# Kernel optimization log

Measured on AMD Instinct MI355X. Metric: run time of the kernel, lower is better.

## Reference

```python
import jax, jax.numpy as jnp
import numpy as np

N_NODES = 8   # chain DAG 0->1->...->7
B = 2048      # n_samples
T_STEPS = 8   # end_wind
Z_DIM = 32    # latent_dim // 2
EMB = 8       # emb_dim
GRU_H = 24
HID = 64


def setup_inputs() -> dict:
    key = jax.random.key(0)
    ks = jax.random.split(key, 20)
    def rn(k, shape, scale=0.1):
        return jax.random.normal(k, shape, jnp.float32) * scale
    return {
        "z": jax.random.normal(ks[0], (N_NODES, B, T_STEPS, Z_DIM), jnp.float32),
        "cond_w1": rn(ks[1], (N_NODES, 32, 1)),
        "cond_b1": rn(ks[2], (N_NODES, 32)),
        "cond_w2": rn(ks[3], (N_NODES, EMB, 32)),
        "cond_b2": rn(ks[4], (N_NODES, EMB)),
        "proj_w": rn(ks[5], (N_NODES, GRU_H, Z_DIM + 2 * EMB)),  # node 0 uses first 40 cols
        "proj_b": rn(ks[6], (N_NODES, GRU_H)),
        "gru_proj_w": rn(ks[7], (GRU_H, GRU_H)),
        "gru_proj_b": rn(ks[8], (GRU_H,)),
        "gru_wih": rn(ks[9], (N_NODES, 2, 3 * GRU_H, GRU_H)),
        "gru_whh": rn(ks[10], (N_NODES, 2, 3 * GRU_H, GRU_H)),
        "gru_bih": rn(ks[11], (N_NODES, 2, 3 * GRU_H)),
        "gru_bhh": rn(ks[12], (N_NODES, 2, 3 * GRU_H)),
        "cm_w1": rn(ks[13], (N_NODES, HID, GRU_H)),
        "cm_b1": rn(ks[14], (N_NODES, HID)),
        "cm_w2": rn(ks[15], (N_NODES, HID, HID)),
        "cm_b2": rn(ks[16], (N_NODES, HID)),
        "cm_w3": rn(ks[17], (N_NODES, 1, HID)),
        "cm_b3": rn(ks[18], (N_NODES, 1)),
        "end_wind": T_STEPS,
    }


def _leaky(x):
    return jnp.where(x >= 0, x, 0.01 * x)  # nn.LeakyReLU default slope


def _gru_layer(x, wih, whh, bih, bhh):
    """torch nn.GRU single layer, batch_first. x: [B, L, H] -> [B, L, H]."""
    h0 = jnp.zeros((x.shape[0], GRU_H), x.dtype)
    def step(h, xt):
        gi = xt @ wih.T + bih            # [B, 3H], gate order r, z, n
        gh = h @ whh.T + bhh
        i_r, i_z, i_n = jnp.split(gi, 3, axis=-1)
        h_r, h_z, h_n = jnp.split(gh, 3, axis=-1)
        r = jax.nn.sigmoid(i_r + h_r)
        zg = jax.nn.sigmoid(i_z + h_z)
        n = jnp.tanh(i_n + r * h_n)
        hn = (1.0 - zg) * n + zg * h
        return hn, hn
    _, ys = jax.lax.scan(step, h0, jnp.swapaxes(x, 0, 1))
    return jnp.swapaxes(ys, 0, 1)


def _forward(z, cond_w1, cond_b1, cond_w2, cond_b2, proj_w, proj_b,
             gru_proj_w, gru_proj_b, gru_wih, gru_whh, gru_bih, gru_bhh,
             cm_w1, cm_b1, cm_w2, cm_b2, cm_w3, cm_b3, end_wind):
    n_nodes, bsz = z.shape[0], z.shape[1]
    dt = z.dtype

    def cond_net(n, x):  # x: [B, L, 1] -> [B, L, EMB]
        h = jax.nn.relu(x @ cond_w1[n].T + cond_b1[n])
        return h @ cond_w2[n].T + cond_b2[n]

    def pipeline(n, z_mod):  # decode_pipeline: proj -> leaky -> gru_proj -> 2-layer GRU -> CausalMap
        w = proj_w[n][:, : z_mod.shape[-1]]
        h = _leaky(z_mod @ w.T + proj_b[n])
        g = h @ gru_proj_w.T + gru_proj_b
        y = _gru_layer(g, gru_wih[n, 0], gru_whh[n, 0], gru_bih[n, 0], gru_bhh[n, 0])
        y = _gru_layer(y, gru_wih[n, 1], gru_whh[n, 1], gru_bih[n, 1], gru_bhh[n, 1])
        d = jax.nn.relu(y @ cm_w1[n].T + cm_b1[n])
        d = jax.nn.relu(d @ cm_w2[n].T + cm_b2[n])
        return d @ cm_w3[n].T + cm_b3[n]  # [B, L, 1]

    decoded = [None] * n_nodes
    reals = [[] for _ in range(n_nodes)]
    for idx in range(end_wind):
        # chain DAG: in-degree grouping (deg 0 = node 0, deg 1 = nodes 1..7 in order)
        # coincides with node order 0..N-1.
        for node in range(n_nodes):
            z_mod = z[node][:, : idx + 1]                       # [B, idx+1, Z_DIM]
            if idx != 0:
                emb_self = cond_net(node, decoded[node])        # [B, idx, EMB]
                emb_self = jnp.concatenate(
                    [emb_self, jnp.zeros((bsz, 1, EMB), dt)], axis=1)
            else:
                emb_self = jnp.zeros((bsz, 1, EMB), dt)
            z_mod = jnp.concatenate([z_mod, emb_self], axis=2)
            if node > 0:  # single predecessor node-1, already decoded this idx
                if idx != 0:
                    emb_p = cond_net(node - 1, decoded[node - 1])  # [B, idx+1, EMB]
                else:
                    emb_p = jnp.zeros((bsz, 1, EMB), dt)
                z_mod = jnp.concatenate([z_mod, emb_p], axis=2)
            d = pipeline(node, z_mod)                           # [B, idx+1, 1]
            decoded[node] = d
            reals[node].append(d[:, idx:idx + 1, 0])
    # [B, T, N]
    return jnp.stack([jnp.concatenate(r, axis=1) for r in reals], axis=-1)


def reference(z, cond_w1, cond_b1, cond_w2, cond_b2, proj_w, proj_b,
              gru_proj_w, gru_proj_b, gru_wih, gru_whh, gru_bih, gru_bhh,
              cm_w1, cm_b1, cm_w2, cm_b2, cm_w3, cm_b3, end_wind):
    return _forward(z, cond_w1, cond_b1, cond_w2, cond_b2, proj_w, proj_b,
                    gru_proj_w, gru_proj_b, gru_wih, gru_whh, gru_bih, gru_bhh,
                    cm_w1, cm_b1, cm_w2, cm_b2, cm_w3, cm_b3, int(end_wind))
```

## Files before the change

kernel.cpp:

```cpp
#include <hip/hip_runtime.h>


#define NT 64
#define SYNC() asm volatile("s_waitcnt lgkmcnt(0)" ::: "memory")

__device__ __forceinline__ float sigm(float x) { return 1.0f / (1.0f + __expf(-x)); }
__device__ __forceinline__ float tanh_fast(float x) {
  x = fminf(15.0f, fmaxf(-15.0f, x));
  float e = __expf(2.0f * x);
  return (e - 1.0f) / (e + 1.0f);
}
__device__ __forceinline__ float leaky(float x) { return x >= 0.0f ? x : 0.01f * x; }

template <int N4>
__device__ __forceinline__ float dotv2(const float* __restrict__ w, const float* h) {
  const float4* w4 = reinterpret_cast<const float4*>(w);
  const float4* h4 = reinterpret_cast<const float4*>(h);
  float a0 = 0.0f, a1 = 0.0f;
#pragma unroll
  for (int i = 0; i < N4; i += 2) {
    float4 x0 = w4[i], y0 = h4[i];
    float4 x1 = w4[i + 1], y1 = h4[i + 1];
    a0 = fmaf(x0.x, y0.x, a0); a0 = fmaf(x0.y, y0.y, a0);
    a0 = fmaf(x0.z, y0.z, a0); a0 = fmaf(x0.w, y0.w, a0);
    a1 = fmaf(x1.x, y1.x, a1); a1 = fmaf(x1.y, y1.y, a1);
    a1 = fmaf(x1.z, y1.z, a1); a1 = fmaf(x1.w, y1.w, a1);
  }
  return a0 + a1;
}

template <int N4>
__device__ __forceinline__ float dotv4(const float* __restrict__ w, const float* h) {
  const float4* w4 = reinterpret_cast<const float4*>(w);
  const float4* h4 = reinterpret_cast<const float4*>(h);
  float a0 = 0.0f, a1 = 0.0f, a2 = 0.0f, a3 = 0.0f;
#pragma unroll
  for (int i = 0; i < N4; i += 4) {
    float4 x0 = w4[i], y0 = h4[i];
    float4 x1 = w4[i + 1], y1 = h4[i + 1];
    float4 x2 = w4[i + 2], y2 = h4[i + 2];
    float4 x3 = w4[i + 3], y3 = h4[i + 3];
    a0 = fmaf(x0.x, y0.x, a0); a0 = fmaf(x0.y, y0.y, a0);
    a0 = fmaf(x0.z, y0.z, a0); a0 = fmaf(x0.w, y0.w, a0);
    a1 = fmaf(x1.x, y1.x, a1); a1 = fmaf(x1.y, y1.y, a1);
    a1 = fmaf(x1.z, y1.z, a1); a1 = fmaf(x1.w, y1.w, a1);
    a2 = fmaf(x2.x, y2.x, a2); a2 = fmaf(x2.y, y2.y, a2);
    a2 = fmaf(x2.z, y2.z, a2); a2 = fmaf(x2.w, y2.w, a2);
    a3 = fmaf(x3.x, y3.x, a3); a3 = fmaf(x3.y, y3.y, a3);
    a3 = fmaf(x3.w, y3.w, a3); a3 = fmaf(x3.z, y3.z, a3);
  }
  return (a0 + a1) + (a2 + a3);
}

__device__ __forceinline__ void load_gates_w(
    const float* __restrict__ wih, const float* __restrict__ bih,
    int lane, int rowB, float4 WA[6], float4 WB[6], float& bA, float& bB) {
  const float4* wa = reinterpret_cast<const float4*>(wih + (size_t)lane * 24);
  const float4* wb = reinterpret_cast<const float4*>(wih + (size_t)rowB * 24);
#pragma unroll
  for (int i = 0; i < 6; ++i) { WA[i] = wa[i]; WB[i] = wb[i]; }
  bA = bih[lane]; bB = bih[rowB];
}

__device__ __forceinline__ void load_rec_w(
    const float* __restrict__ whh, const float* __restrict__ bhh,
    int jq, int half, float4 Wr[3], float4 Wz[3], float4 Wn[3],
    float& bR, float& bZ, float& bN) {
  const float4* wr = reinterpret_cast<const float4*>(whh + jq * 24 + half * 12);
  const float4* wz = reinterpret_cast<const float4*>(whh + (24 + jq) * 24 + half * 12);
  const float4* wn = reinterpret_cast<const float4*>(whh + (48 + jq) * 24 + half * 12);
#pragma unroll
  for (int i = 0; i < 3; ++i) { Wr[i] = wr[i]; Wz[i] = wz[i]; Wn[i] = wn[i]; }
  bR = half ? 0.0f : bhh[jq];
  bZ = half ? 0.0f : bhh[24 + jq];
  bN = half ? 0.0f : bhh[48 + jq];
}

__device__ __forceinline__ void gates_comp(
    const float4 WA[6], const float4 WB[6], float bA, float bB,
    const float* srcp, float* s_gi, int L, int lane) {
  int t = 0;
#pragma unroll 1
  for (; t + 1 < L; t += 2) {
    const float4* h0 = reinterpret_cast<const float4*>(srcp + t * 24);
    const float4* h1 = reinterpret_cast<const float4*>(srcp + t * 24 + 24);
    float a0 = bA, a1 = bA, c0 = bB, c1 = bB;
#pragma unroll
    for (int i = 0; i < 6; ++i) {
      float4 p = h0[i], q = h1[i], A = WA[i], Bv = WB[i];
      a0 = fmaf(A.x, p.x, a0); a0 = fmaf(A.y, p.y, a0);
      a0 = fmaf(A.z, p.z, a0); a0 = fmaf(A.w, p.w, a0);
      a1 = fmaf(A.x, q.x, a1); a1 = fmaf(A.y, q.y, a1);
      a1 = fmaf(A.z, q.z, a1); a1 = fmaf(A.w, q.w, a1);
      c0 = fmaf(Bv.x, p.x, c0); c0 = fmaf(Bv.y, p.y, c0);
      c0 = fmaf(Bv.z, p.z, c0); c0 = fmaf(Bv.w, p.w, c0);
      c1 = fmaf(Bv.x, q.x, c1); c1 = fmaf(Bv.y, q.y, c1);
      c1 = fmaf(Bv.z, q.z, c1); c1 = fmaf(Bv.w, q.w, c1);
    }
    s_gi[t * 72 + lane] = a0;
    s_gi[t * 72 + 72 + lane] = a1;
    if (lane < 8) {
      s_gi[t * 72 + 64 + lane] = c0;
      s_gi[t * 72 + 136 + lane] = c1;
    }
  }
  if (t < L) {
    const float4* h0 = reinterpret_cast<const float4*>(srcp + t * 24);
    float a0 = bA, c0 = bB;
#pragma unroll
    for (int i = 0; i < 6; ++i) {
      float4 p = h0[i], A = WA[i], Bv = WB[i];
      a0 = fmaf(A.x, p.x, a0); a0 = fmaf(A.y, p.y, a0);
      a0 = fmaf(A.z, p.z, a0); a0 = fmaf(A.w, p.w, a0);
      c0 = fmaf(Bv.x, p.x, c0); c0 = fmaf(Bv.y, p.y, c0);
      c0 = fmaf(Bv.z, p.z, c0); c0 = fmaf(Bv.w, p.w, c0);
    }
    s_gi[t * 72 + lane] = a0;
    if (lane < 8) s_gi[t * 72 + 64 + lane] = c0;
  }
}

__device__ __forceinline__ void rec_comp(
    const float4 Wr[3], const float4 Wz[3], const float4 Wn[3],
    float bR, float bZ, float bN,
    const float* s_gi, float* s_hid, float* s_y, int L, int lane, int jq, int half) {
  if (lane < 24) s_hid[lane] = 0.0f;
  int cur = 0;
#pragma unroll 1
  for (int t = 0; t < L; ++t) {
    const float4* hp = reinterpret_cast<const float4*>(s_hid + cur * 24 + half * 12);
    float gr = bR, gz = bZ, gn = bN;
#pragma unroll
    for (int i = 0; i < 3; ++i) {
      float4 hh = hp[i];
      gr = fmaf(Wr[i].x, hh.x, gr); gr = fmaf(Wr[i].y, hh.y, gr);
      gr = fmaf(Wr[i].z, hh.z, gr); gr = fmaf(Wr[i].w, hh.w, gr);
      gz = fmaf(Wz[i].x, hh.x, gz); gz = fmaf(Wz[i].y, hh.y, gz);
      gz = fmaf(Wz[i].z, hh.z, gz); gz = fmaf(Wz[i].w, hh.w, gz);
      gn = fmaf(Wn[i].x, hh.x, gn); gn = fmaf(Wn[i].y, hh.y, gn);
      gn = fmaf(Wn[i].z, hh.z, gn); gn = fmaf(Wn[i].w, hh.w, gn);
    }
    gr += __shfl_xor(gr, 32);
    gz += __shfl_xor(gz, 32);
    gn += __shfl_xor(gn, 32);
    const float* gi = s_gi + t * 72;
    float r   = sigm(gi[jq] + gr);
    float zg  = sigm(gi[24 + jq] + gz);
    float nn2 = tanh_fast(gi[48 + jq] + r * gn);
    float hold = s_hid[cur * 24 + jq];
    float hnew = fmaf(zg, hold - nn2, nn2);
    if (lane < 24) {
      s_hid[(cur ^ 1) * 24 + lane] = hnew;
      s_y[t * 24 + lane] = hnew;
    }
    cur ^= 1;
  }
}

__global__ __launch_bounds__(NT, 2) void tcm_kernel(
    const float* __restrict__ z,
    const float* __restrict__ cond_w1, const float* __restrict__ cond_b1,
    const float* __restrict__ cond_w2, const float* __restrict__ cond_b2,
    const float* __restrict__ proj_w, const float* __restrict__ proj_b,
    const float* __restrict__ gpw, const float* __restrict__ gpb,
    const float* __restrict__ gru_wih, const float* __restrict__ gru_whh,
    const float* __restrict__ gru_bih, const float* __restrict__ gru_bhh,
    const float* __restrict__ cm_w1, const float* __restrict__ cm_b1,
    const float* __restrict__ cm_w2, const float* __restrict__ cm_b2,
    const float* __restrict__ cm_w3, const float* __restrict__ cm_b3,
    const int* __restrict__ endw,
    float* __restrict__ out, int Btot) {
  __shared__ __align__(16) float lds[3488];
  float* s_x   = lds;
  float* s_h   = lds + 384;
  float* s_g   = lds + 576;
  float* s_gi  = lds + 768;
  float* s_y   = lds + 1344;
  float* s_hid = lds + 1536;
  float* s_d1  = lds + 1584;
  float* s_d2  = lds + 2128;
  float* s_dd  = lds + 2672;
  float* s_ch  = lds + 2688;
  float* s_emb = lds + 2976;

  const int lane = threadIdx.x;
  const int b = blockIdx.x;
  const int T = endw[0];
  const int jm = lane & 31;
  const int half = lane >> 5;
  const int jq = jm < 24 ? jm : 0;
  const int rowB = 64 + (lane & 7);

#pragma unroll 1
  for (int idx = 0; idx < T; ++idx) {
    const int L = idx + 1;
#pragma unroll 1
    for (int n = 0; n < 8; ++n) {
      const float* wih0 = gru_wih + (size_t)(n * 2) * 1728;
      const float* wih1 = wih0 + 1728;
      const float* whh0 = gru_whh + (size_t)(n * 2) * 1728;
      const float* whh1 = whh0 + 1728;
      const float* bih0 = gru_bih + (n * 2) * 72;
      const float* bih1 = bih0 + 72;
      const float* bhh0 = gru_bhh + (n * 2) * 72;
      const float* bhh1 = bhh0 + 72;

      float4 WA[6], WB[6]; float bA, bB;
      load_gates_w(wih0, bih0, lane, rowB, WA, WB, bA, bB);

      if (lane < L * 8) {
        const float4* z4 = reinterpret_cast<const float4*>(
            z + ((size_t)n * Btot + b) * 8 * 32);
        int t = lane >> 3, q = lane & 7;
        reinterpret_cast<float4*>(s_x)[t * 12 + q] = z4[t * 8 + q];
      }
#pragma unroll 1
      for (int it = lane; it < L * 16; it += NT) {
        int t = it >> 4, c = it & 15;
        float v = 0.0f;
        if (c < 8) {
          if (t < idx) v = s_emb[n * 64 + t * 8 + c];
        } else {
          if (n > 0 && idx > 0) v = s_emb[(n - 1) * 64 + t * 8 + (c - 8)];
        }
        s_x[t * 48 + 32 + c] = v;
      }
      SYNC();
#pragma unroll 1
      for (int it = lane; it < L * 24; it += NT) {
        int t = it / 24, j = it - t * 24;
        float acc = proj_b[n * 24 + j] +
                    dotv2<12>(proj_w + (size_t)(n * 24 + j) * 48, s_x + t * 48);
        s_h[t * 24 + j] = leaky(acc);
      }
      SYNC();
#pragma unroll 1
      for (int it = lane; it < L * 24; it += NT) {
        int t = it / 24, j = it - t * 24;
        s_g[t * 24 + j] = gpb[j] + dotv2<6>(gpw + j * 24, s_h + t * 24);
      }
      SYNC();
      float4 Wr[3], Wz[3], Wn[3]; float bR, bZ, bN;
      load_rec_w(whh0, bhh0, jq, half, Wr, Wz, Wn, bR, bZ, bN);
      gates_comp(WA, WB, bA, bB, s_g, s_gi, L, lane);
      SYNC();
      float4 WA1[6], WB1[6]; float bA1, bB1;
      load_gates_w(wih1, bih1, lane, rowB, WA1, WB1, bA1, bB1);
      rec_comp(Wr, Wz, Wn, bR, bZ, bN, s_gi, s_hid, s_y, L, lane, jq, half);
      SYNC();
      float4 Wr1[3], Wz1[3], Wn1[3]; float bR1, bZ1, bN1;
      load_rec_w(whh1, bhh1, jq, half, Wr1, Wz1, Wn1, bR1, bZ1, bN1);
      gates_comp(WA1, WB1, bA1, bB1, s_y, s_gi, L, lane);
      SYNC();
      float4 C1[6];
      {
        const float4* p = reinterpret_cast<const float4*>(
            cm_w1 + (size_t)(n * 64 + lane) * 24);
#pragma unroll
        for (int i = 0; i < 6; ++i) C1[i] = p[i];
      }
      const float c1b = cm_b1[n * 64 + lane];
      rec_comp(Wr1, Wz1, Wn1, bR1, bZ1, bN1, s_gi, s_hid, s_y, L, lane, jq, half);
      SYNC();
      float4 C2[16];
      {
        const float4* p = reinterpret_cast<const float4*>(
            cm_w2 + (size_t)(n * 64 + lane) * 64);
#pragma unroll
        for (int i = 0; i < 16; ++i) C2[i] = p[i];
      }
      const float c2b = cm_b2[n * 64 + lane];
      {
        int t = 0;
#pragma unroll 1
        for (; t + 1 < L; t += 2) {
          const float4* y0 = reinterpret_cast<const float4*>(s_y + t * 24);
          const float4* y1 = reinterpret_cast<const float4*>(s_y + t * 24 + 24);
          float a0 = c1b, a1 = c1b;
#pragma unroll
          for (int i = 0; i < 6; ++i) {
            float4 pp = y0[i], q = y1[i], W = C1[i];
            a0 = fmaf(W.x, pp.x, a0); a0 = fmaf(W.y, pp.y, a0);
            a0 = fmaf(W.z, pp.z, a0); a0 = fmaf(W.w, pp.w, a0);
            a1 = fmaf(W.x, q.x, a1); a1 = fmaf(W.y, q.y, a1);
            a1 = fmaf(W.z, q.z, a1); a1 = fmaf(W.w, q.w, a1);
          }
          s_d1[t * 68 + lane] = fmaxf(a0, 0.0f);
          s_d1[t * 68 + 68 + lane] = fmaxf(a1, 0.0f);
        }
        if (t < L) {
          float acc = c1b;
          const float4* y0 = reinterpret_cast<const float4*>(s_y + t * 24);
#pragma unroll
          for (int i = 0; i < 6; ++i) {
            float4 pp = y0[i], W = C1[i];
            acc = fmaf(W.x, pp.x, acc); acc = fmaf(W.y, pp.y, acc);
            acc = fmaf(W.z, pp.z, acc); acc = fmaf(W.w, pp.w, acc);
          }
          s_d1[t * 68 + lane] = fmaxf(acc, 0.0f);
        }
      }
      SYNC();
      {
        int t = 0;
#pragma unroll 1
        for (; t + 1 < L; t += 2) {
          const float4* d0 = reinterpret_cast<const float4*>(s_d1 + t * 68);
          const float4* d1 = reinterpret_cast<const float4*>(s_d1 + t * 68 + 68);
          float a0 = c2b, a1 = 0.0f, c0 = c2b, c1 = 0.0f;
#pragma unroll
          for (int i = 0; i < 16; i += 2) {
            float4 W0 = C2[i], W1 = C2[i + 1];
            float4 p0 = d0[i], p1 = d0[i + 1], q0 = d1[i], q1 = d1[i + 1];
            a0 = fmaf(W0.x, p0.x, a0); a0 = fmaf(W0.y, p0.y, a0);
            a0 = fmaf(W0.z, p0.z, a0); a0 = fmaf(W0.w, p0.w, a0);
            a1 = fmaf(W1.x, p1.x, a1); a1 = fmaf(W1.y, p1.y, a1);
            a1 = fmaf(W1.z, p1.z, a1); a1 = fmaf(W1.w, p1.w, a1);
            c0 = fmaf(W0.x, q0.x, c0); c0 = fmaf(W0.y, q0.y, c0);
            c0 = fmaf(W0.z, q0.z, c0); c0 = fmaf(W0.w, q0.w, c0);
            c1 = fmaf(W1.x, q1.x, c1); c1 = fmaf(W1.y, q1.y, c1);
            c1 = fmaf(W1.z, q1.z, c1); c1 = fmaf(W1.w, q1.w, c1);
          }
          s_d2[t * 68 + lane] = fmaxf(a0 + a1, 0.0f);
          s_d2[t * 68 + 68 + lane] = fmaxf(c0 + c1, 0.0f);
        }
        if (t < L) {
          const float4* d0 = reinterpret_cast<const float4*>(s_d1 + t * 68);
          float a0 = c2b, a1 = 0.0f;
#pragma unroll
          for (int i = 0; i < 16; i += 2) {
            float4 W0 = C2[i], W1 = C2[i + 1];
            float4 p0 = d0[i], p1 = d0[i + 1];
            a0 = fmaf(W0.x, p0.x, a0); a0 = fmaf(W0.y, p0.y, a0);
            a0 = fmaf(W0.z, p0.z, a0); a0 = fmaf(W0.w, p0.w, a0);
            a1 = fmaf(W1.x, p1.x, a1); a1 = fmaf(W1.y, p1.y, a1);
            a1 = fmaf(W1.z, p1.z, a1); a1 = fmaf(W1.w, p1.w, a1);
          }
          s_d2[t * 68 + lane] = fmaxf(a0 + a1, 0.0f);
        }
      }
      SYNC();
      if (lane < L) {
        int t = lane;
        float dv = cm_b3[n] + dotv4<16>(cm_w3 + n * 64, s_d2 + t * 68);
        s_dd[t] = dv;
        if (t == idx)
          out[((size_t)b * T + idx) * 8 + n] = dv;
      }
      SYNC();
#pragma unroll 1
      for (int it = lane; it < L * 32; it += NT) {
        int t = it >> 5, k = it & 31;
        s_ch[t * 36 + k] =
            fmaxf(fmaf(s_dd[t], cond_w1[n * 32 + k], cond_b1[n * 32 + k]), 0.0f);
      }
      SYNC();
      if (lane < L * 8) {
        int t = lane >> 3, c = lane & 7;
        s_emb[n * 64 + t * 8 + c] =
            cond_b2[n * 8 + c] +
            dotv2<8>(cond_w2 + (size_t)(n * 8 + c) * 32, s_ch + t * 36);
      }
      SYNC();
    }
  }
}

extern "C" void kernel_launch(void* const* d_in, const int* in_sizes, int n_in,
                              void* d_out, int out_size, void* d_ws, size_t ws_size,
                              hipStream_t stream) {
  const float* z       = (const float*)d_in[0];
  const float* cond_w1 = (const float*)d_in[1];
  const float* cond_b1 = (const float*)d_in[2];
  const float* cond_w2 = (const float*)d_in[3];
  const float* cond_b2 = (const float*)d_in[4];
  const float* proj_w  = (const float*)d_in[5];
  const float* proj_b  = (const float*)d_in[6];
  const float* gpw     = (const float*)d_in[7];
  const float* gpb     = (const float*)d_in[8];
  const float* gru_wih = (const float*)d_in[9];
  const float* gru_whh = (const float*)d_in[10];
  const float* gru_bih = (const float*)d_in[11];
  const float* gru_bhh = (const float*)d_in[12];
  const float* cm_w1   = (const float*)d_in[13];
  const float* cm_b1   = (const float*)d_in[14];
  const float* cm_w2   = (const float*)d_in[15];
  const float* cm_b2   = (const float*)d_in[16];
  const float* cm_w3   = (const float*)d_in[17];
  const float* cm_b3   = (const float*)d_in[18];
  const int*   endw    = (const int*)d_in[19];
  float* out = (float*)d_out;

  int Btot = in_sizes[0] / (8 * 8 * 32);

  tcm_kernel<<<Btot, NT, 0, stream>>>(
      z, cond_w1, cond_b1, cond_w2, cond_b2, proj_w, proj_b, gpw, gpb,
      gru_wih, gru_whh, gru_bih, gru_bhh, cm_w1, cm_b1, cm_w2, cm_b2,
      cm_w3, cm_b3, endw, out, Btot);
}
```

Before: 1.026 ms.

## Process two samples per wavefront with one GRU recurrence per half-wave

Each 64-lane block now handles two batch samples, each with its own LDS region. The weight-stationary dense layers (projection, gate inputs, MLP) are computed for both samples at once so every loaded weight register is reused twice. The GRU recurrence drops the cross-half shuffle reduction: each 32-lane half computes full 24-wide dot products for its own sample. This halves the block count and raises register pressure (launch bounds lowered to 1 block per SIMD), which trades occupancy for weight reuse and fewer shuffles.

```diff
diff --git a/kernel.cpp b/kernel.cpp
--- a/kernel.cpp
+++ b/kernel.cpp
@@ -3,6 +3,19 @@
 
 #define NT 64
 #define SYNC() asm volatile("s_waitcnt lgkmcnt(0)" ::: "memory")
+
+#define SS   3488
+#define OX   0
+#define OH   384
+#define OG   576
+#define OGI  768
+#define OY   1344
+#define OHID 1536
+#define OD1  1584
+#define OD2  2128
+#define ODD  2672
+#define OCH  2688
+#define OEMB 2976
 
 __device__ __forceinline__ float sigm(float x) { return 1.0f / (1.0f + __expf(-x)); }
 __device__ __forceinline__ float tanh_fast(float x) {
@@ -47,9 +60,35 @@
     a2 = fmaf(x2.x, y2.x, a2); a2 = fmaf(x2.y, y2.y, a2);
     a2 = fmaf(x2.z, y2.z, a2); a2 = fmaf(x2.w, y2.w, a2);
     a3 = fmaf(x3.x, y3.x, a3); a3 = fmaf(x3.y, y3.y, a3);
-    a3 = fmaf(x3.w, y3.w, a3); a3 = fmaf(x3.z, y3.z, a3);
+    a3 = fmaf(x3.z, y3.z, a3); a3 = fmaf(x3.w, y3.w, a3);
   }
   return (a0 + a1) + (a2 + a3);
+}
+
+template <int N4>
+__device__ __forceinline__ void dot2_dual(const float* __restrict__ w,
+                                          const float* hA, const float* hB,
+                                          float& ra, float& rb) {
+  const float4* w4 = reinterpret_cast<const float4*>(w);
+  const float4* a4 = reinterpret_cast<const float4*>(hA);
+  const float4* b4 = reinterpret_cast<const float4*>(hB);
+  float a0 = 0.0f, a1 = 0.0f, b0 = 0.0f, b1 = 0.0f;
+#pragma unroll
+  for (int i = 0; i < N4; i += 2) {
+    float4 w0 = w4[i], w1 = w4[i + 1];
+    float4 x0 = a4[i], x1 = a4[i + 1];
+    float4 y0 = b4[i], y1 = b4[i + 1];
+    a0 = fmaf(w0.x, x0.x, a0); a0 = fmaf(w0.y, x0.y, a0);
+    a0 = fmaf(w0.z, x0.z, a0); a0 = fmaf(w0.w, x0.w, a0);
+    a1 = fmaf(w1.x, x1.x, a1); a1 = fmaf(w1.y, x1.y, a1);
+    a1 = fmaf(w1.z, x1.z, a1); a1 = fmaf(w1.w, x1.w, a1);
+    b0 = fmaf(w0.x, y0.x, b0); b0 = fmaf(w0.y, y0.y, b0);
+    b0 = fmaf(w0.z, y0.z, b0); b0 = fmaf(w0.w, y0.w, b0);
+    b1 = fmaf(w1.x, y1.x, b1); b1 = fmaf(w1.y, y1.y, b1);
+    b1 = fmaf(w1.z, y1.z, b1); b1 = fmaf(w1.w, y1.w, b1);
+  }
+  ra = a0 + a1;
+  rb = b0 + b1;
 }
 
 __device__ __forceinline__ void load_gates_w(
@@ -63,31 +102,27 @@
 }
 
 __device__ __forceinline__ void load_rec_w(
-    const float* __restrict__ whh, const float* __restrict__ bhh,
-    int jq, int half, float4 Wr[3], float4 Wz[3], float4 Wn[3],
-    float& bR, float& bZ, float& bN) {
-  const float4* wr = reinterpret_cast<const float4*>(whh + jq * 24 + half * 12);
-  const float4* wz = reinterpret_cast<const float4*>(whh + (24 + jq) * 24 + half * 12);
-  const float4* wn = reinterpret_cast<const float4*>(whh + (48 + jq) * 24 + half * 12);
-#pragma unroll
-  for (int i = 0; i < 3; ++i) { Wr[i] = wr[i]; Wz[i] = wz[i]; Wn[i] = wn[i]; }
-  bR = half ? 0.0f : bhh[jq];
-  bZ = half ? 0.0f : bhh[24 + jq];
-  bN = half ? 0.0f : bhh[48 + jq];
-}
-
-__device__ __forceinline__ void gates_comp(
+    const float* __restrict__ whh, const float* __restrict__ bhh, int jq,
+    float4 Wr[6], float4 Wz[6], float4 Wn[6], float& bR, float& bZ, float& bN) {
+  const float4* wr = reinterpret_cast<const float4*>(whh + jq * 24);
+  const float4* wz = reinterpret_cast<const float4*>(whh + (24 + jq) * 24);
+  const float4* wn = reinterpret_cast<const float4*>(whh + (48 + jq) * 24);
+#pragma unroll
+  for (int i = 0; i < 6; ++i) { Wr[i] = wr[i]; Wz[i] = wz[i]; Wn[i] = wn[i]; }
+  bR = bhh[jq]; bZ = bhh[24 + jq]; bN = bhh[48 + jq];
+}
+
+__device__ __forceinline__ void gates_dual(
     const float4 WA[6], const float4 WB[6], float bA, float bB,
-    const float* srcp, float* s_gi, int L, int lane) {
-  int t = 0;
-#pragma unroll 1
-  for (; t + 1 < L; t += 2) {
-    const float4* h0 = reinterpret_cast<const float4*>(srcp + t * 24);
-    const float4* h1 = reinterpret_cast<const float4*>(srcp + t * 24 + 24);
+    const float* g0, const float* g1, float* gi0, float* gi1, int L, int lane) {
+#pragma unroll 1
+  for (int t = 0; t < L; ++t) {
+    const float4* p4 = reinterpret_cast<const float4*>(g0 + t * 24);
+    const float4* q4 = reinterpret_cast<const float4*>(g1 + t * 24);
     float a0 = bA, a1 = bA, c0 = bB, c1 = bB;
 #pragma unroll
     for (int i = 0; i < 6; ++i) {
-      float4 p = h0[i], q = h1[i], A = WA[i], Bv = WB[i];
+      float4 p = p4[i], q = q4[i], A = WA[i], Bv = WB[i];
       a0 = fmaf(A.x, p.x, a0); a0 = fmaf(A.y, p.y, a0);
       a0 = fmaf(A.z, p.z, a0); a0 = fmaf(A.w, p.w, a0);
       a1 = fmaf(A.x, q.x, a1); a1 = fmaf(A.y, q.y, a1);
@@ -97,41 +132,26 @@
       c1 = fmaf(Bv.x, q.x, c1); c1 = fmaf(Bv.y, q.y, c1);
       c1 = fmaf(Bv.z, q.z, c1); c1 = fmaf(Bv.w, q.w, c1);
     }
-    s_gi[t * 72 + lane] = a0;
-    s_gi[t * 72 + 72 + lane] = a1;
+    gi0[t * 72 + lane] = a0;
+    gi1[t * 72 + lane] = a1;
     if (lane < 8) {
-      s_gi[t * 72 + 64 + lane] = c0;
-      s_gi[t * 72 + 136 + lane] = c1;
+      gi0[t * 72 + 64 + lane] = c0;
+      gi1[t * 72 + 64 + lane] = c1;
     }
   }
-  if (t < L) {
-    const float4* h0 = reinterpret_cast<const float4*>(srcp + t * 24);
-    float a0 = bA, c0 = bB;
+}
+
+__device__ __forceinline__ void rec_grp(
+    const float4 Wr[6], const float4 Wz[6], const float4 Wn[6],
+    float bR, float bZ, float bN, float* sb, int L, int jm, int jq) {
+  if (jm < 24) sb[OHID + jm] = 0.0f;
+  int cur = 0;
+#pragma unroll 1
+  for (int t = 0; t < L; ++t) {
+    const float4* hp = reinterpret_cast<const float4*>(sb + OHID + cur * 24);
+    float gr = bR, gz = bZ, gn = bN;
 #pragma unroll
     for (int i = 0; i < 6; ++i) {
-      float4 p = h0[i], A = WA[i], Bv = WB[i];
-      a0 = fmaf(A.x, p.x, a0); a0 = fmaf(A.y, p.y, a0);
-      a0 = fmaf(A.z, p.z, a0); a0 = fmaf(A.w, p.w, a0);
-      c0 = fmaf(Bv.x, p.x, c0); c0 = fmaf(Bv.y, p.y, c0);
-      c0 = fmaf(Bv.z, p.z, c0); c0 = fmaf(Bv.w, p.w, c0);
-    }
-    s_gi[t * 72 + lane] = a0;
-    if (lane < 8) s_gi[t * 72 + 64 + lane] = c0;
-  }
-}
-
-__device__ __forceinline__ void rec_comp(
-    const float4 Wr[3], const float4 Wz[3], const float4 Wn[3],
-    float bR, float bZ, float bN,
-    const float* s_gi, float* s_hid, float* s_y, int L, int lane, int jq, int half) {
-  if (lane < 24) s_hid[lane] = 0.0f;
-  int cur = 0;
-#pragma unroll 1
-  for (int t = 0; t < L; ++t) {
-    const float4* hp = reinterpret_cast<const float4*>(s_hid + cur * 24 + half * 12);
-    float gr = bR, gz = bZ, gn = bN;
-#pragma unroll
-    for (int i = 0; i < 3; ++i) {
       float4 hh = hp[i];
       gr = fmaf(Wr[i].x, hh.x, gr); gr = fmaf(Wr[i].y, hh.y, gr);
       gr = fmaf(Wr[i].z, hh.z, gr); gr = fmaf(Wr[i].w, hh.w, gr);
@@ -140,24 +160,21 @@
       gn = fmaf(Wn[i].x, hh.x, gn); gn = fmaf(Wn[i].y, hh.y, gn);
       gn = fmaf(Wn[i].z, hh.z, gn); gn = fmaf(Wn[i].w, hh.w, gn);
     }
-    gr += __shfl_xor(gr, 32);
-    gz += __shfl_xor(gz, 32);
-    gn += __shfl_xor(gn, 32);
-    const float* gi = s_gi + t * 72;
+    const float* gi = sb + OGI + t * 72;
     float r   = sigm(gi[jq] + gr);
     float zg  = sigm(gi[24 + jq] + gz);
     float nn2 = tanh_fast(gi[48 + jq] + r * gn);
-    float hold = s_hid[cur * 24 + jq];
+    float hold = sb[OHID + cur * 24 + jq];
     float hnew = fmaf(zg, hold - nn2, nn2);
-    if (lane < 24) {
-      s_hid[(cur ^ 1) * 24 + lane] = hnew;
-      s_y[t * 24 + lane] = hnew;
+    if (jm < 24) {
+      sb[OHID + (cur ^ 1) * 24 + jm] = hnew;
+      sb[OY + t * 24 + jm] = hnew;
     }
     cur ^= 1;
   }
 }
 
-__global__ __launch_bounds__(NT, 2) void tcm_kernel(
+__global__ __launch_bounds__(NT, 1) void tcm_kernel(
     const float* __restrict__ z,
     const float* __restrict__ cond_w1, const float* __restrict__ cond_b1,
     const float* __restrict__ cond_w2, const float* __restrict__ cond_b2,
@@ -170,26 +187,23 @@
     const float* __restrict__ cm_w3, const float* __restrict__ cm_b3,
     const int* __restrict__ endw,
     float* __restrict__ out, int Btot) {
-  __shared__ __align__(16) float lds[3488];
-  float* s_x   = lds;
-  float* s_h   = lds + 384;
-  float* s_g   = lds + 576;
-  float* s_gi  = lds + 768;
-  float* s_y   = lds + 1344;
-  float* s_hid = lds + 1536;
-  float* s_d1  = lds + 1584;
-  float* s_d2  = lds + 2128;
-  float* s_dd  = lds + 2672;
-  float* s_ch  = lds + 2688;
-  float* s_emb = lds + 2976;
+  __shared__ __align__(16) float lds[2 * SS];
+  float* Ls0 = lds;
+  float* Ls1 = lds + SS;
 
   const int lane = threadIdx.x;
-  const int b = blockIdx.x;
+  const int jm   = lane & 31;
+  const int grp  = lane >> 5;
+  const int jq   = jm < 24 ? jm : 0;
+  const int rowB = 64 + (lane & 7);
   const int T = endw[0];
-  const int jm = lane & 31;
-  const int half = lane >> 5;
-  const int jq = jm < 24 ? jm : 0;
-  const int rowB = 64 + (lane & 7);
+
+  const int b0 = 2 * blockIdx.x;
+  const int b1 = b0 + 1;
+  const bool b1ok = (b1 < Btot);
+  const int b1c = b1ok ? b1 : (Btot - 1);
+  float* myb = lds + grp * SS;
+  const int bs = grp ? b1c : b0;
 
 #pragma unroll 1
   for (int idx = 0; idx < T; ++idx) {
@@ -208,49 +222,58 @@
       float4 WA[6], WB[6]; float bA, bB;
       load_gates_w(wih0, bih0, lane, rowB, WA, WB, bA, bB);
 
-      if (lane < L * 8) {
+      {
         const float4* z4 = reinterpret_cast<const float4*>(
-            z + ((size_t)n * Btot + b) * 8 * 32);
-        int t = lane >> 3, q = lane & 7;
-        reinterpret_cast<float4*>(s_x)[t * 12 + q] = z4[t * 8 + q];
-      }
-#pragma unroll 1
-      for (int it = lane; it < L * 16; it += NT) {
-        int t = it >> 4, c = it & 15;
-        float v = 0.0f;
-        if (c < 8) {
-          if (t < idx) v = s_emb[n * 64 + t * 8 + c];
-        } else {
-          if (n > 0 && idx > 0) v = s_emb[(n - 1) * 64 + t * 8 + (c - 8)];
+            z + ((size_t)n * Btot + bs) * 256);
+        float4* x4 = reinterpret_cast<float4*>(myb + OX);
+#pragma unroll 1
+        for (int it = jm; it < L * 8; it += 32) {
+          int t = it >> 3, q = it & 7;
+          x4[t * 12 + q] = z4[t * 8 + q];
         }
-        s_x[t * 48 + 32 + c] = v;
+#pragma unroll 1
+        for (int it = jm; it < L * 16; it += 32) {
+          int t = it >> 4, c = it & 15;
+          float v = 0.0f;
+          if (c < 8) {
+            if (t < idx) v = myb[OEMB + n * 64 + t * 8 + c];
+          } else {
+            if (n > 0 && idx > 0) v = myb[OEMB + (n - 1) * 64 + t * 8 + (c - 8)];
+          }
+          myb[OX + t * 48 + 32 + c] = v;
+        }
       }
       SYNC();
 #pragma unroll 1
       for (int it = lane; it < L * 24; it += NT) {
         int t = it / 24, j = it - t * 24;
-        float acc = proj_b[n * 24 + j] +
-                    dotv2<12>(proj_w + (size_t)(n * 24 + j) * 48, s_x + t * 48);
-        s_h[t * 24 + j] = leaky(acc);
+        float ra, rb;
+        dot2_dual<12>(proj_w + (size_t)(n * 24 + j) * 48,
+                      Ls0 + OX + t * 48, Ls1 + OX + t * 48, ra, rb);
+        float pb = proj_b[n * 24 + j];
+        Ls0[OH + t * 24 + j] = leaky(pb + ra);
+        Ls1[OH + t * 24 + j] = leaky(pb + rb);
       }
       SYNC();
 #pragma unroll 1
       for (int it = lane; it < L * 24; it += NT) {
         int t = it / 24, j = it - t * 24;
-        s_g[t * 24 + j] = gpb[j] + dotv2<6>(gpw + j * 24, s_h + t * 24);
-      }
-      SYNC();
-      float4 Wr[3], Wz[3], Wn[3]; float bR, bZ, bN;
-      load_rec_w(whh0, bhh0, jq, half, Wr, Wz, Wn, bR, bZ, bN);
-      gates_comp(WA, WB, bA, bB, s_g, s_gi, L, lane);
-      SYNC();
-      float4 WA1[6], WB1[6]; float bA1, bB1;
-      load_gates_w(wih1, bih1, lane, rowB, WA1, WB1, bA1, bB1);
-      rec_comp(Wr, Wz, Wn, bR, bZ, bN, s_gi, s_hid, s_y, L, lane, jq, half);
-      SYNC();
-      float4 Wr1[3], Wz1[3], Wn1[3]; float bR1, bZ1, bN1;
-      load_rec_w(whh1, bhh1, jq, half, Wr1, Wz1, Wn1, bR1, bZ1, bN1);
-      gates_comp(WA1, WB1, bA1, bB1, s_y, s_gi, L, lane);
+        float ra, rb;
+        dot2_dual<6>(gpw + j * 24, Ls0 + OH + t * 24, Ls1 + OH + t * 24, ra, rb);
+        float gb = gpb[j];
+        Ls0[OG + t * 24 + j] = gb + ra;
+        Ls1[OG + t * 24 + j] = gb + rb;
+      }
+      SYNC();
+      float4 Wr[6], Wz[6], Wn[6]; float bR, bZ, bN;
+      load_rec_w(whh0, bhh0, jq, Wr, Wz, Wn, bR, bZ, bN);
+      gates_dual(WA, WB, bA, bB, Ls0 + OG, Ls1 + OG, Ls0 + OGI, Ls1 + OGI, L, lane);
+      SYNC();
+      load_gates_w(wih1, bih1, lane, rowB, WA, WB, bA, bB);
+      rec_grp(Wr, Wz, Wn, bR, bZ, bN, myb, L, jm, jq);
+      SYNC();
+      load_rec_w(whh1, bhh1, jq, Wr, Wz, Wn, bR, bZ, bN);
+      gates_dual(WA, WB, bA, bB, Ls0 + OY, Ls1 + OY, Ls0 + OGI, Ls1 + OGI, L, lane);
       SYNC();
       float4 C1[6];
       {
@@ -260,106 +283,82 @@
         for (int i = 0; i < 6; ++i) C1[i] = p[i];
       }
       const float c1b = cm_b1[n * 64 + lane];
-      rec_comp(Wr1, Wz1, Wn1, bR1, bZ1, bN1, s_gi, s_hid, s_y, L, lane, jq, half);
-      SYNC();
-      float4 C2[16];
+      rec_grp(Wr, Wz, Wn, bR, bZ, bN, myb, L, jm, jq);
+      SYNC();
+#pragma unroll 1
+      for (int t = 0; t < L; ++t) {
+        const float4* p4 = reinterpret_cast<const float4*>(Ls0 + OY + t * 24);
+        const float4* q4 = reinterpret_cast<const float4*>(Ls1 + OY + t * 24);
+        float a0 = c1b, a1 = 0.0f, d0 = c1b, d1 = 0.0f;
+#pragma unroll
+        for (int i = 0; i < 6; i += 2) {
+          float4 w0 = C1[i], w1 = C1[i + 1];
+          float4 p0 = p4[i], p1 = p4[i + 1], q0 = q4[i], q1 = q4[i + 1];
+          a0 = fmaf(w0.x, p0.x, a0); a0 = fmaf(w0.y, p0.y, a0);
+          a0 = fmaf(w0.z, p0.z, a0); a0 = fmaf(w0.w, p0.w, a0);
+          a1 = fmaf(w1.x, p1.x, a1); a1 = fmaf(w1.y, p1.y, a1);
+          a1 = fmaf(w1.z, p1.z, a1); a1 = fmaf(w1.w, p1.w, a1);
+          d0 = fmaf(w0.x, q0.x, d0); d0 = fmaf(w0.y, q0.y, d0);
+          d0 = fmaf(w0.z, q0.z, d0); d0 = fmaf(w0.w, q0.w, d0);
+          d1 = fmaf(w1.x, q1.x, d1); d1 = fmaf(w1.y, q1.y, d1);
+          d1 = fmaf(w1.z, q1.z, d1); d1 = fmaf(w1.w, q1.w, d1);
+        }
+        Ls0[OD1 + t * 68 + lane] = fmaxf(a0 + a1, 0.0f);
+        Ls1[OD1 + t * 68 + lane] = fmaxf(d0 + d1, 0.0f);
+      }
+      SYNC();
       {
-        const float4* p = reinterpret_cast<const float4*>(
+        float4 C2[16];
+        const float4* p2 = reinterpret_cast<const float4*>(
             cm_w2 + (size_t)(n * 64 + lane) * 64);
 #pragma unroll
-        for (int i = 0; i < 16; ++i) C2[i] = p[i];
-      }
-      const float c2b = cm_b2[n * 64 + lane];
-      {
-        int t = 0;
-#pragma unroll 1
-        for (; t + 1 < L; t += 2) {
-          const float4* y0 = reinterpret_cast<const float4*>(s_y + t * 24);
-          const float4* y1 = reinterpret_cast<const float4*>(s_y + t * 24 + 24);
-          float a0 = c1b, a1 = c1b;
-#pragma unroll
-          for (int i = 0; i < 6; ++i) {
-            float4 pp = y0[i], q = y1[i], W = C1[i];
-            a0 = fmaf(W.x, pp.x, a0); a0 = fmaf(W.y, pp.y, a0);
-            a0 = fmaf(W.z, pp.z, a0); a0 = fmaf(W.w, pp.w, a0);
-            a1 = fmaf(W.x, q.x, a1); a1 = fmaf(W.y, q.y, a1);
-            a1 = fmaf(W.z, q.z, a1); a1 = fmaf(W.w, q.w, a1);
+        for (int i = 0; i < 16; ++i) C2[i] = p2[i];
+        const float c2b = cm_b2[n * 64 + lane];
+#pragma unroll 1
+        for (int t = 0; t < L; ++t) {
+          const float4* p4 = reinterpret_cast<const float4*>(Ls0 + OD1 + t * 68);
+          const float4* q4 = reinterpret_cast<const float4*>(Ls1 + OD1 + t * 68);
+          float a0 = c2b, a1 = 0.0f, d0 = c2b, d1 = 0.0f;
+#pragma unroll
+          for (int i = 0; i < 16; i += 2) {
+            float4 w0 = C2[i], w1 = C2[i + 1];
+            float4 p0 = p4[i], p1 = p4[i + 1], q0 = q4[i], q1 = q4[i + 1];
+            a0 = fmaf(w0.x, p0.x, a0); a0 = fmaf(w0.y, p0.y, a0);
+            a0 = fmaf(w0.z, p0.z, a0); a0 = fmaf(w0.w, p0.w, a0);
+            a1 = fmaf(w1.x, p1.x, a1); a1 = fmaf(w1.y, p1.y, a1);
+            a1 = fmaf(w1.z, p1.z, a1); a1 = fmaf(w1.w, p1.w, a1);
+            d0 = fmaf(w0.x, q0.x, d0); d0 = fmaf(w0.y, q0.y, d0);
+            d0 = fmaf(w0.z, q0.z, d0); d0 = fmaf(w0.w, q0.w, d0);
+            d1 = fmaf(w1.x, q1.x, d1); d1 = fmaf(w1.y, q1.y, d1);
+            d1 = fmaf(w1.z, q1.z, d1); d1 = fmaf(w1.w, q1.w, d1);
           }
-          s_d1[t * 68 + lane] = fmaxf(a0, 0.0f);
-          s_d1[t * 68 + 68 + lane] = fmaxf(a1, 0.0f);
+          Ls0[OD2 + t * 68 + lane] = fmaxf(a0 + a1, 0.0f);
+          Ls1[OD2 + t * 68 + lane] = fmaxf(d0 + d1, 0.0f);
         }
-        if (t < L) {
-          float acc = c1b;
-          const float4* y0 = reinterpret_cast<const float4*>(s_y + t * 24);
-#pragma unroll
-          for (int i = 0; i < 6; ++i) {
-            float4 pp = y0[i], W = C1[i];
-            acc = fmaf(W.x, pp.x, acc); acc = fmaf(W.y, pp.y, acc);
-            acc = fmaf(W.z, pp.z, acc); acc = fmaf(W.w, pp.w, acc);
-          }
-          s_d1[t * 68 + lane] = fmaxf(acc, 0.0f);
-        }
-      }
-      SYNC();
-      {
-        int t = 0;
-#pragma unroll 1
-        for (; t + 1 < L; t += 2) {
-          const float4* d0 = reinterpret_cast<const float4*>(s_d1 + t * 68);
-          const float4* d1 = reinterpret_cast<const float4*>(s_d1 + t * 68 + 68);
-          float a0 = c2b, a1 = 0.0f, c0 = c2b, c1 = 0.0f;
-#pragma unroll
-          for (int i = 0; i < 16; i += 2) {
-            float4 W0 = C2[i], W1 = C2[i + 1];
-            float4 p0 = d0[i], p1 = d0[i + 1], q0 = d1[i], q1 = d1[i + 1];
-            a0 = fmaf(W0.x, p0.x, a0); a0 = fmaf(W0.y, p0.y, a0);
-            a0 = fmaf(W0.z, p0.z, a0); a0 = fmaf(W0.w, p0.w, a0);
-            a1 = fmaf(W1.x, p1.x, a1); a1 = fmaf(W1.y, p1.y, a1);
-            a1 = fmaf(W1.z, p1.z, a1); a1 = fmaf(W1.w, p1.w, a1);
-            c0 = fmaf(W0.x, q0.x, c0); c0 = fmaf(W0.y, q0.y, c0);
-            c0 = fmaf(W0.z, q0.z, c0); c0 = fmaf(W0.w, q0.w, c0);
-            c1 = fmaf(W1.x, q1.x, c1); c1 = fmaf(W1.y, q1.y, c1);
-            c1 = fmaf(W1.z, q1.z, c1); c1 = fmaf(W1.w, q1.w, c1);
-          }
-          s_d2[t * 68 + lane] = fmaxf(a0 + a1, 0.0f);
-          s_d2[t * 68 + 68 + lane] = fmaxf(c0 + c1, 0.0f);
-        }
-        if (t < L) {
-          const float4* d0 = reinterpret_cast<const float4*>(s_d1 + t * 68);
-          float a0 = c2b, a1 = 0.0f;
-#pragma unroll
-          for (int i = 0; i < 16; i += 2) {
-            float4 W0 = C2[i], W1 = C2[i + 1];
-            float4 p0 = d0[i], p1 = d0[i + 1];
-            a0 = fmaf(W0.x, p0.x, a0); a0 = fmaf(W0.y, p0.y, a0);
-            a0 = fmaf(W0.z, p0.z, a0); a0 = fmaf(W0.w, p0.w, a0);
-            a1 = fmaf(W1.x, p1.x, a1); a1 = fmaf(W1.y, p1.y, a1);
-            a1 = fmaf(W1.z, p1.z, a1); a1 = fmaf(W1.w, p1.w, a1);
-          }
-          s_d2[t * 68 + lane] = fmaxf(a0 + a1, 0.0f);
-        }
-      }
-      SYNC();
-      if (lane < L) {
-        int t = lane;
-        float dv = cm_b3[n] + dotv4<16>(cm_w3 + n * 64, s_d2 + t * 68);
-        s_dd[t] = dv;
-        if (t == idx)
-          out[((size_t)b * T + idx) * 8 + n] = dv;
-      }
-      SYNC();
-#pragma unroll 1
-      for (int it = lane; it < L * 32; it += NT) {
+      }
+      SYNC();
+      if (jm < L) {
+        int t = jm;
+        float dv = cm_b3[n] + dotv4<16>(cm_w3 + n * 64, myb + OD2 + t * 68);
+        myb[ODD + t] = dv;
+        if (t == idx && (grp == 0 || b1ok))
+          out[((size_t)bs * T + idx) * 8 + n] = dv;
+      }
+      SYNC();
+#pragma unroll 1
+      for (int it = jm; it < L * 32; it += 32) {
         int t = it >> 5, k = it & 31;
-        s_ch[t * 36 + k] =
-            fmaxf(fmaf(s_dd[t], cond_w1[n * 32 + k], cond_b1[n * 32 + k]), 0.0f);
-      }
-      SYNC();
-      if (lane < L * 8) {
-        int t = lane >> 3, c = lane & 7;
-        s_emb[n * 64 + t * 8 + c] =
+        myb[OCH + t * 36 + k] =
+            fmaxf(fmaf(myb[ODD + t], cond_w1[n * 32 + k], cond_b1[n * 32 + k]),
+                  0.0f);
+      }
+      SYNC();
+#pragma unroll 1
+      for (int it = jm; it < L * 8; it += 32) {
+        int t = it >> 3, c = it & 7;
+        myb[OEMB + n * 64 + t * 8 + c] =
             cond_b2[n * 8 + c] +
-            dotv2<8>(cond_w2 + (size_t)(n * 8 + c) * 32, s_ch + t * 36);
+            dotv2<8>(cond_w2 + (size_t)(n * 8 + c) * 32, myb + OCH + t * 36);
       }
       SYNC();
     }
@@ -392,8 +391,9 @@
   float* out = (float*)d_out;
 
   int Btot = in_sizes[0] / (8 * 8 * 32);
-
-  tcm_kernel<<<Btot, NT, 0, stream>>>(
+  int nblocks = (Btot + 1) / 2;
+
+  tcm_kernel<<<nblocks, NT, 0, stream>>>(
       z, cond_w1, cond_b1, cond_w2, cond_b2, proj_w, proj_b, gpw, gpb,
       gru_wih, gru_whh, gru_bih, gru_bhh, cm_w1, cm_b1, cm_w2, cm_b2,
       cm_w3, cm_b3, endw, out, Btot);
```

Measured after the change: 1.064 ms. 3.7% more time.

## Fuse GRU input-gate projection into recurrence loop with one-step lookahead

Applied to the files above, without the earlier changes.

Replaces the separate input-gate pass plus recurrence pass with a fused loop. Each step computes the input gates for the next timestep alongside the current hidden-state update, so independent FMA work can fill the latency of the serial recurrence, and one barrier per layer goes away. Layer-1 weights now reuse the layer-0 register arrays instead of being held in separate ones. Launch bounds are relaxed from 2 to 1 waves per EU, which allows more registers but may lower occupancy.

```diff
diff --git a/kernel.cpp b/kernel.cpp
--- a/kernel.cpp
+++ b/kernel.cpp
@@ -47,7 +47,7 @@
     a2 = fmaf(x2.x, y2.x, a2); a2 = fmaf(x2.y, y2.y, a2);
     a2 = fmaf(x2.z, y2.z, a2); a2 = fmaf(x2.w, y2.w, a2);
     a3 = fmaf(x3.x, y3.x, a3); a3 = fmaf(x3.y, y3.y, a3);
-    a3 = fmaf(x3.w, y3.w, a3); a3 = fmaf(x3.z, y3.z, a3);
+    a3 = fmaf(x3.z, y3.z, a3); a3 = fmaf(x3.w, y3.w, a3);
   }
   return (a0 + a1) + (a2 + a3);
 }
@@ -76,58 +76,37 @@
   bN = half ? 0.0f : bhh[48 + jq];
 }
 
-__device__ __forceinline__ void gates_comp(
+__device__ __forceinline__ void gates_row(
     const float4 WA[6], const float4 WB[6], float bA, float bB,
-    const float* srcp, float* s_gi, int L, int lane) {
-  int t = 0;
-#pragma unroll 1
-  for (; t + 1 < L; t += 2) {
-    const float4* h0 = reinterpret_cast<const float4*>(srcp + t * 24);
-    const float4* h1 = reinterpret_cast<const float4*>(srcp + t * 24 + 24);
-    float a0 = bA, a1 = bA, c0 = bB, c1 = bB;
-#pragma unroll
-    for (int i = 0; i < 6; ++i) {
-      float4 p = h0[i], q = h1[i], A = WA[i], Bv = WB[i];
-      a0 = fmaf(A.x, p.x, a0); a0 = fmaf(A.y, p.y, a0);
-      a0 = fmaf(A.z, p.z, a0); a0 = fmaf(A.w, p.w, a0);
-      a1 = fmaf(A.x, q.x, a1); a1 = fmaf(A.y, q.y, a1);
-      a1 = fmaf(A.z, q.z, a1); a1 = fmaf(A.w, q.w, a1);
-      c0 = fmaf(Bv.x, p.x, c0); c0 = fmaf(Bv.y, p.y, c0);
-      c0 = fmaf(Bv.z, p.z, c0); c0 = fmaf(Bv.w, p.w, c0);
-      c1 = fmaf(Bv.x, q.x, c1); c1 = fmaf(Bv.y, q.y, c1);
-      c1 = fmaf(Bv.z, q.z, c1); c1 = fmaf(Bv.w, q.w, c1);
-    }
-    s_gi[t * 72 + lane] = a0;
-    s_gi[t * 72 + 72 + lane] = a1;
-    if (lane < 8) {
-      s_gi[t * 72 + 64 + lane] = c0;
-      s_gi[t * 72 + 136 + lane] = c1;
-    }
-  }
-  if (t < L) {
-    const float4* h0 = reinterpret_cast<const float4*>(srcp + t * 24);
-    float a0 = bA, c0 = bB;
-#pragma unroll
-    for (int i = 0; i < 6; ++i) {
-      float4 p = h0[i], A = WA[i], Bv = WB[i];
-      a0 = fmaf(A.x, p.x, a0); a0 = fmaf(A.y, p.y, a0);
-      a0 = fmaf(A.z, p.z, a0); a0 = fmaf(A.w, p.w, a0);
-      c0 = fmaf(Bv.x, p.x, c0); c0 = fmaf(Bv.y, p.y, c0);
-      c0 = fmaf(Bv.z, p.z, c0); c0 = fmaf(Bv.w, p.w, c0);
-    }
-    s_gi[t * 72 + lane] = a0;
-    if (lane < 8) s_gi[t * 72 + 64 + lane] = c0;
-  }
-}
-
-__device__ __forceinline__ void rec_comp(
+    const float* src_row, float* gi_row, int lane) {
+  const float4* h0 = reinterpret_cast<const float4*>(src_row);
+  float a0 = bA, c0 = bB;
+#pragma unroll
+  for (int i = 0; i < 6; ++i) {
+    float4 p = h0[i], A = WA[i], Bv = WB[i];
+    a0 = fmaf(A.x, p.x, a0); a0 = fmaf(A.y, p.y, a0);
+    a0 = fmaf(A.z, p.z, a0); a0 = fmaf(A.w, p.w, a0);
+    c0 = fmaf(Bv.x, p.x, c0); c0 = fmaf(Bv.y, p.y, c0);
+    c0 = fmaf(Bv.z, p.z, c0); c0 = fmaf(Bv.w, p.w, c0);
+  }
+  gi_row[lane] = a0;
+  if (lane < 8) gi_row[64 + lane] = c0;
+}
+
+__device__ __forceinline__ void fused_gates_rec(
+    const float4 WA[6], const float4 WB[6], float bA, float bB,
     const float4 Wr[3], const float4 Wz[3], const float4 Wn[3],
     float bR, float bZ, float bN,
-    const float* s_gi, float* s_hid, float* s_y, int L, int lane, int jq, int half) {
+    const float* srcp, float* s_gi, float* s_hid, float* s_y,
+    int L, int lane, int jq, int half) {
+  gates_row(WA, WB, bA, bB, srcp, s_gi, lane);
   if (lane < 24) s_hid[lane] = 0.0f;
+  SYNC();
   int cur = 0;
 #pragma unroll 1
   for (int t = 0; t < L; ++t) {
+    if (t + 1 < L)
+      gates_row(WA, WB, bA, bB, srcp + (t + 1) * 24, s_gi + (t + 1) * 72, lane);
     const float4* hp = reinterpret_cast<const float4*>(s_hid + cur * 24 + half * 12);
     float gr = bR, gz = bZ, gn = bN;
 #pragma unroll
@@ -157,7 +136,7 @@
   }
 }
 
-__global__ __launch_bounds__(NT, 2) void tcm_kernel(
+__global__ __launch_bounds__(NT, 1) void tcm_kernel(
     const float* __restrict__ z,
     const float* __restrict__ cond_w1, const float* __restrict__ cond_b1,
     const float* __restrict__ cond_w2, const float* __restrict__ cond_b2,
@@ -242,16 +221,11 @@
       SYNC();
       float4 Wr[3], Wz[3], Wn[3]; float bR, bZ, bN;
       load_rec_w(whh0, bhh0, jq, half, Wr, Wz, Wn, bR, bZ, bN);
-      gates_comp(WA, WB, bA, bB, s_g, s_gi, L, lane);
-      SYNC();
-      float4 WA1[6], WB1[6]; float bA1, bB1;
-      load_gates_w(wih1, bih1, lane, rowB, WA1, WB1, bA1, bB1);
-      rec_comp(Wr, Wz, Wn, bR, bZ, bN, s_gi, s_hid, s_y, L, lane, jq, half);
-      SYNC();
-      float4 Wr1[3], Wz1[3], Wn1[3]; float bR1, bZ1, bN1;
-      load_rec_w(whh1, bhh1, jq, half, Wr1, Wz1, Wn1, bR1, bZ1, bN1);
-      gates_comp(WA1, WB1, bA1, bB1, s_y, s_gi, L, lane);
-      SYNC();
+      fused_gates_rec(WA, WB, bA, bB, Wr, Wz, Wn, bR, bZ, bN,
+                      s_g, s_gi, s_hid, s_y, L, lane, jq, half);
+      SYNC();
+      load_gates_w(wih1, bih1, lane, rowB, WA, WB, bA, bB);
+      load_rec_w(whh1, bhh1, jq, half, Wr, Wz, Wn, bR, bZ, bN);
       float4 C1[6];
       {
         const float4* p = reinterpret_cast<const float4*>(
@@ -260,7 +234,8 @@
         for (int i = 0; i < 6; ++i) C1[i] = p[i];
       }
       const float c1b = cm_b1[n * 64 + lane];
-      rec_comp(Wr1, Wz1, Wn1, bR1, bZ1, bN1, s_gi, s_hid, s_y, L, lane, jq, half);
+      fused_gates_rec(WA, WB, bA, bB, Wr, Wz, Wn, bR, bZ, bN,
+                      s_y, s_gi, s_hid, s_y, L, lane, jq, half);
       SYNC();
       float4 C2[16];
       {
```

Result: slower. 1.048 ms (+2.2%).

## Fold GRU input projection into layer-0 weights and cache z projection across windows

Applied to the files above, without the earlier changes.

A small pre-kernel multiplies the GRU projection matrix into each node's layer-0 input weights and bias, so the separate gru_proj linear pass and its sync disappear from the per-node loop. The z-part of the input projection, which does not depend on the decode index, is now computed once at idx==0 for all 8 timesteps and kept in LDS. Later windows only add the 16 embedding columns. This removes repeated dot products and global z loads, but raises LDS use, which could lower occupancy, and adds an extra launch plus a workspace dependency.

```diff
diff --git a/kernel.cpp b/kernel.cpp
--- a/kernel.cpp
+++ b/kernel.cpp
@@ -157,31 +157,57 @@
   }
 }
 
+__global__ void fuse_kernel(const float* __restrict__ gru_wih,
+                            const float* __restrict__ gru_bih,
+                            const float* __restrict__ gpw,
+                            const float* __restrict__ gpb,
+                            float* __restrict__ fw, float* __restrict__ fb) {
+  const int n = blockIdx.x;
+  const int tid = threadIdx.x;
+  const float* w = gru_wih + (size_t)(n * 2) * 1728;
+  for (int it = tid; it < 1728; it += 64) {
+    int r = it / 24, k = it - r * 24;
+    float acc = 0.0f;
+#pragma unroll
+    for (int j = 0; j < 24; ++j) acc = fmaf(w[r * 24 + j], gpw[j * 24 + k], acc);
+    fw[(size_t)n * 1728 + it] = acc;
+  }
+  if (tid < 72 + 0) {
+    for (int r = tid; r < 72; r += 64) {
+      float acc = gru_bih[(n * 2) * 72 + r];
+#pragma unroll
+      for (int j = 0; j < 24; ++j) acc = fmaf(w[r * 24 + j], gpb[j], acc);
+      fb[n * 72 + r] = acc;
+    }
+  }
+}
+
 __global__ __launch_bounds__(NT, 2) void tcm_kernel(
     const float* __restrict__ z,
     const float* __restrict__ cond_w1, const float* __restrict__ cond_b1,
     const float* __restrict__ cond_w2, const float* __restrict__ cond_b2,
     const float* __restrict__ proj_w, const float* __restrict__ proj_b,
-    const float* __restrict__ gpw, const float* __restrict__ gpb,
     const float* __restrict__ gru_wih, const float* __restrict__ gru_whh,
     const float* __restrict__ gru_bih, const float* __restrict__ gru_bhh,
     const float* __restrict__ cm_w1, const float* __restrict__ cm_b1,
     const float* __restrict__ cm_w2, const float* __restrict__ cm_b2,
     const float* __restrict__ cm_w3, const float* __restrict__ cm_b3,
     const int* __restrict__ endw,
+    const float* __restrict__ fw, const float* __restrict__ fb,
     float* __restrict__ out, int Btot) {
-  __shared__ __align__(16) float lds[3488];
-  float* s_x   = lds;
-  float* s_h   = lds + 384;
-  float* s_g   = lds + 576;
-  float* s_gi  = lds + 768;
-  float* s_y   = lds + 1344;
-  float* s_hid = lds + 1536;
-  float* s_d1  = lds + 1584;
-  float* s_d2  = lds + 2128;
-  float* s_dd  = lds + 2672;
-  float* s_ch  = lds + 2688;
-  float* s_emb = lds + 2976;
+  __shared__ __align__(16) float lds[4832];
+  float* s_e   = lds;
+  float* s_h   = lds + 128;
+  float* s_gi  = lds + 320;
+  float* s_y   = lds + 896;
+  float* s_hid = lds + 1088;
+  float* s_d1  = lds + 1136;
+  float* s_d2  = lds + 1680;
+  float* s_dd  = lds + 2224;
+  float* s_ch  = lds + 2240;
+  float* s_emb = lds + 2528;
+  float* s_pz  = lds + 3040;
+  float* s_zz  = lds + 4576;
 
   const int lane = threadIdx.x;
   const int b = blockIdx.x;
@@ -196,23 +222,28 @@
     const int L = idx + 1;
 #pragma unroll 1
     for (int n = 0; n < 8; ++n) {
-      const float* wih0 = gru_wih + (size_t)(n * 2) * 1728;
-      const float* wih1 = wih0 + 1728;
+      const float* wih1 = gru_wih + (size_t)(n * 2 + 1) * 1728;
       const float* whh0 = gru_whh + (size_t)(n * 2) * 1728;
       const float* whh1 = whh0 + 1728;
-      const float* bih0 = gru_bih + (n * 2) * 72;
-      const float* bih1 = bih0 + 72;
+      const float* bih1 = gru_bih + (n * 2 + 1) * 72;
       const float* bhh0 = gru_bhh + (n * 2) * 72;
       const float* bhh1 = bhh0 + 72;
 
       float4 WA[6], WB[6]; float bA, bB;
-      load_gates_w(wih0, bih0, lane, rowB, WA, WB, bA, bB);
-
-      if (lane < L * 8) {
+      load_gates_w(fw + (size_t)n * 1728, fb + n * 72, lane, rowB, WA, WB, bA, bB);
+
+      if (idx == 0) {
         const float4* z4 = reinterpret_cast<const float4*>(
             z + ((size_t)n * Btot + b) * 8 * 32);
-        int t = lane >> 3, q = lane & 7;
-        reinterpret_cast<float4*>(s_x)[t * 12 + q] = z4[t * 8 + q];
+        reinterpret_cast<float4*>(s_zz)[lane] = z4[lane];
+        SYNC();
+#pragma unroll 1
+        for (int it = lane; it < 192; it += NT) {
+          int t = it / 24, j = it - t * 24;
+          s_pz[n * 192 + t * 24 + j] =
+              proj_b[n * 24 + j] +
+              dotv2<8>(proj_w + (size_t)(n * 24 + j) * 48, s_zz + t * 32);
+        }
       }
 #pragma unroll 1
       for (int it = lane; it < L * 16; it += NT) {
@@ -223,26 +254,20 @@
         } else {
           if (n > 0 && idx > 0) v = s_emb[(n - 1) * 64 + t * 8 + (c - 8)];
         }
-        s_x[t * 48 + 32 + c] = v;
+        s_e[t * 16 + c] = v;
       }
       SYNC();
 #pragma unroll 1
       for (int it = lane; it < L * 24; it += NT) {
         int t = it / 24, j = it - t * 24;
-        float acc = proj_b[n * 24 + j] +
-                    dotv2<12>(proj_w + (size_t)(n * 24 + j) * 48, s_x + t * 48);
+        float acc = s_pz[n * 192 + t * 24 + j] +
+                    dotv2<4>(proj_w + (size_t)(n * 24 + j) * 48 + 32, s_e + t * 16);
         s_h[t * 24 + j] = leaky(acc);
-      }
-      SYNC();
-#pragma unroll 1
-      for (int it = lane; it < L * 24; it += NT) {
-        int t = it / 24, j = it - t * 24;
-        s_g[t * 24 + j] = gpb[j] + dotv2<6>(gpw + j * 24, s_h + t * 24);
       }
       SYNC();
       float4 Wr[3], Wz[3], Wn[3]; float bR, bZ, bN;
       load_rec_w(whh0, bhh0, jq, half, Wr, Wz, Wn, bR, bZ, bN);
-      gates_comp(WA, WB, bA, bB, s_g, s_gi, L, lane);
+      gates_comp(WA, WB, bA, bB, s_h, s_gi, L, lane);
       SYNC();
       float4 WA1[6], WB1[6]; float bA1, bB1;
       load_gates_w(wih1, bih1, lane, rowB, WA1, WB1, bA1, bB1);
@@ -393,8 +418,13 @@
 
   int Btot = in_sizes[0] / (8 * 8 * 32);
 
+  float* fw = (float*)d_ws;
+  float* fb = fw + 8 * 1728;
+
+  fuse_kernel<<<8, 64, 0, stream>>>(gru_wih, gru_bih, gpw, gpb, fw, fb);
+
   tcm_kernel<<<Btot, NT, 0, stream>>>(
-      z, cond_w1, cond_b1, cond_w2, cond_b2, proj_w, proj_b, gpw, gpb,
+      z, cond_w1, cond_b1, cond_w2, cond_b2, proj_w, proj_b,
       gru_wih, gru_whh, gru_bih, gru_bhh, cm_w1, cm_b1, cm_w2, cm_b2,
-      cm_w3, cm_b3, endw, out, Btot);
-}
+      cm_w3, cm_b3, endw, fw, fb, out, Btot);
+}
```

Measured after the change: 870.5 us. 1.18x faster.
